# Optimization experiments

Hardware: AMD Instinct MI355X
Metric: run time of the kernel (lower is better)

Reference implementation:

```python
import jax, jax.numpy as jnp
import numpy as np
from jax import lax

WS = 11
CH = 3
DENOM_G = 2 * 0.2 ** 2
DENOM_L = 2 * 0.2 ** 2
C1 = 0.01 ** 2
C2 = 0.03 ** 2


def _make_window(ws=WS, channel=CH):
    sigma = ws / 6.0
    x = np.arange(ws) - ws // 2
    g = np.exp(-(x ** 2) / (2.0 * sigma ** 2))
    g = g / g.sum()
    w2 = np.outer(g, g)  # [ws, ws]
    w = np.broadcast_to(w2, (1, channel, ws, ws)) / channel  # sum over channels, averaged
    return jnp.asarray(w, dtype=jnp.float32)


def _wconv(x, window):
    # x: [N, C, H, W] -> [N, 1, H, W], SAME padding (ws odd)
    pad = WS // 2
    return lax.conv_general_dilated(
        x, window, window_strides=(1, 1), padding=[(pad, pad), (pad, pad)],
        dimension_numbers=("NCHW", "OIHW", "NCHW"))


def setup_inputs() -> dict:
    key = jax.random.key(0)
    k1, k2 = jax.random.split(key)
    X = jax.random.uniform(k1, (1, CH, 2048, 2048), dtype=jnp.float32)
    Ys = jax.random.uniform(k2, (4, CH, 2048, 2048), dtype=jnp.float32)
    return {"X": X, "Ys": Ys}


def reference(X, Ys):
    K, C, H, W = Ys.shape
    window = _make_window(WS, C)

    muY_seq = _wconv(Ys, window).reshape(K, H, W)
    sigmaY_sq_seq = _wconv(Ys * Ys, window).reshape(K, H, W) - muY_seq * muY_seq
    patch_index = jnp.argmax(sigmaY_sq_seq, axis=0)  # [H, W]

    muX = _wconv(X, window).reshape(H, W)
    muX_sq = muX * muX
    sigmaX_sq = _wconv(X * X, window).reshape(H, W) - muX_sq
    sigmaXY = _wconv(X * Ys, window).reshape(K, H, W) - muX[None] * muY_seq

    cs_seq = (2 * sigmaXY + C2) / (sigmaX_sq[None] + sigmaY_sq_seq + C2)  # [K, H, W]
    cs_map = jnp.take_along_axis(cs_seq, patch_index[None], axis=0)[0]  # [H, W]

    # is_lum=True luminance component
    lY = jnp.mean(muY_seq.reshape(K, -1), axis=1)  # [K]
    lL = jnp.exp(-((muY_seq - 0.5) ** 2) / DENOM_L)  # [K, H, W]
    lG = jnp.exp(-((lY - 0.5) ** 2) / DENOM_G)[:, None, None]  # [K, 1, 1]
    LY = lG * lL
    muY = jnp.sum(LY * muY_seq, axis=0) / jnp.sum(LY, axis=0)  # [H, W]
    l_map = (2 * muX * muY + C1) / (muX_sq + muY * muY + C1)

    q = jnp.mean(l_map * cs_map)
    return q
```

## Files before the change

kernel.cpp:

```cpp
#include <hip/hip_runtime.h>
#include <math.h>

#define HH 2048
#define WW 2048
#define PLANE 4194304
#define TPITCH 44
#define TPP (26*TPITCH)


__device__ inline double wave_red(double v) {
#pragma unroll
  for (int o = 32; o > 0; o >>= 1) v += __shfl_down(v, o, 64);
  return v;
}

__global__ void k0_window(float* gwin, float* gwin3) {
  if (threadIdx.x == 0) {
    double e[11], s = 0.0;
    double sig = 11.0 / 6.0;
    for (int i = 0; i < 11; ++i) {
      double x = (double)(i - 5);
      e[i] = exp(-(x * x) / (2.0 * sig * sig));
      s += e[i];
    }
    for (int i = 0; i < 11; ++i) {
      gwin[i]  = (float)(e[i] / s);
      gwin3[i] = (float)(e[i] / (3.0 * s));
    }
  }
}

__global__ __launch_bounds__(256) void k1_lY(const float* __restrict__ Ys,
                                             const float* __restrict__ gwin,
                                             double* __restrict__ lYpart) {
  int bid = blockIdx.x;
  int tid = threadIdx.x;
  double acc = 0.0;
  __shared__ float P[12];
  __shared__ double red[4];

  if (bid < 2048) {
    const float4* __restrict__ p = (const float4*)Ys;
    int base = bid * 6144 + tid;
#pragma unroll 1
    for (int gblk = 0; gblk < 3; ++gblk) {
      float ax = 0.f, ay = 0.f;
#pragma unroll
      for (int u = 0; u < 8; ++u) {
        float4 v = p[base + (gblk * 8 + u) * 256];
        ax += v.x + v.z;
        ay += v.y + v.w;
      }
      acc += (double)(ax + ay);
    }
  } else {
    int b = bid - 2048;
    int k = b >> 4, sub = b & 15;
    if (tid == 0) {
      float s = 0.f;
      for (int i = 0; i < 12; ++i) { P[i] = s; if (i < 11) s += gwin[i]; }
    }
    __syncthreads();
    const float4* __restrict__ Yk4 = (const float4*)(Ys + (size_t)k * 3 * PLANE);
    auto covP = [&](int r) -> float {
      if (r >= 5 && r <= 2042) return 1.0f;
      int dhi = r + 5; if (dhi > 10) dhi = 10;
      int dlo = r - 2042; if (dlo < 0) dlo = 0;
      return P[dhi + 1] - P[dlo];
    };
#pragma unroll 1
    for (int t = sub * 256 + tid; t < 39816; t += 4096) {
      int ch, row, g4;
      if (t < 15360) {
        ch = t / 5120;
        int r = (t % 5120) / 512;
        g4 = t & 511;
        row = (r < 5) ? r : r + 2038;
      } else {
        int u = t - 15360;
        ch = u / 8152;
        int rem = u % 8152;
        row = 5 + (rem >> 2);
        int gi = rem & 3;
        g4 = (gi < 2) ? gi : 508 + gi;
      }
      float4 v = Yk4[ch * 1048576 + row * 512 + g4];
      float cy = covP(row);
      int x0 = g4 << 2;
      float w0 = cy * covP(x0)     - 1.0f;
      float w1 = cy * covP(x0 + 1) - 1.0f;
      float w2 = cy * covP(x0 + 2) - 1.0f;
      float w3 = cy * covP(x0 + 3) - 1.0f;
      acc += (double)(w0 * v.x + w1 * v.y + w2 * v.z + w3 * v.w);
    }
  }

  acc = wave_red(acc);
  int lane = tid & 63, wid = tid >> 6;
  if (bid >= 2048 && tid == 0) {}
  __syncthreads();
  if (lane == 0) red[wid] = acc;
  __syncthreads();
  if (tid == 0) {
    double tot = red[0] + red[1] + red[2] + red[3];
    if (bid < 2048) {
      int k = bid >> 9;
      lYpart[k * 528 + (bid & 511)] = tot;
    } else {
      int b = bid - 2048;
      lYpart[(b >> 4) * 528 + 512 + (b & 15)] = tot;
    }
  }
}

__global__ __launch_bounds__(256) void k2a_lG(const double* __restrict__ lYpart,
                                              double* __restrict__ lG) {
  __shared__ double red[4];
  for (int k = 0; k < 4; ++k) {
    const double* p = lYpart + k * 528;
    double v = p[threadIdx.x] + p[256 + threadIdx.x];
    if (threadIdx.x < 16) v += p[512 + threadIdx.x];
    v = wave_red(v);
    int lane = threadIdx.x & 63, wid = threadIdx.x >> 6;
    if (lane == 0) red[wid] = v;
    __syncthreads();
    if (threadIdx.x == 0) {
      double tot = red[0] + red[1] + red[2] + red[3];
      double lY = tot * (1.0 / 12582912.0);
      double d = lY - 0.5;
      lG[k] = exp(-(d * d) / 0.08);
    }
    __syncthreads();
  }
}

__global__ __launch_bounds__(512, 4) void k2_main(const float* __restrict__ X,
                                                  const float* __restrict__ Ys,
                                                  const float* __restrict__ gwin,
                                                  const float* __restrict__ gwin3,
                                                  const double* __restrict__ lG,
                                                  double* __restrict__ qpart) {
  __shared__ float4 lds4[(4 + 14 * TPP) / 4];
  __shared__ double qred[8];
  float* prod = (float*)lds4 + 4;

  int bid = blockIdx.x;
  int wg = (bid & 7) * 1024 + (bid >> 3);
  int tX = wg & 63, tY = wg >> 6;
  int x0 = tX * 32, y0 = tY * 16;
  int tid = threadIdx.x;

  float g[11], g3[11];
#pragma unroll
  for (int i = 0; i < 11; ++i) { g[i] = gwin[i]; g3[i] = gwin3[i]; }

  if (tid < 286) {
    int row = tid / 11, g4 = tid - row * 11;
    int gy = y0 - 5 + row;
    int gx = x0 - 6 + g4 * 4;
    bool rok = (unsigned)gy < (unsigned)HH;
    size_t rbase = (size_t)gy * WW;
    float v[15][4];
#pragma unroll
    for (int p = 0; p < 15; ++p) {
      const float* src = (p < 3) ? (X + (size_t)p * PLANE)
                                 : (Ys + (size_t)(p - 3) * PLANE);
#pragma unroll
      for (int h = 0; h < 2; ++h) {
        int xx = gx + 2 * h;
        float2 w2 = make_float2(0.f, 0.f);
        if (rok && (unsigned)xx < (unsigned)WW)
          w2 = *(const float2*)(src + rbase + xx);
        v[p][2 * h] = w2.x;
        v[p][2 * h + 1] = w2.y;
      }
    }
    int ob = row * TPITCH + g4 * 4;
    {
      float4 a, b2;
#pragma unroll
      for (int e = 0; e < 4; ++e) {
        float s0 = v[0][e], s1 = v[1][e], s2 = v[2][e];
        ((float*)&a)[e]  = s0 + s1 + s2;
        ((float*)&b2)[e] = s0 * s0 + s1 * s1 + s2 * s2;
      }
      *(float4*)(prod + 0 * TPP + ob) = a;
      *(float4*)(prod + 1 * TPP + ob) = b2;
#pragma unroll
      for (int k = 0; k < 4; ++k) {
        float4 sy, sy2, sxy;
#pragma unroll
        for (int e = 0; e < 4; ++e) {
          float ya = v[3 + 3 * k][e], yb = v[4 + 3 * k][e], yc = v[5 + 3 * k][e];
          ((float*)&sy)[e]  = ya + yb + yc;
          ((float*)&sy2)[e] = ya * ya + yb * yb + yc * yc;
          ((float*)&sxy)[e] = v[0][e] * ya + v[1][e] * yb + v[2][e] * yc;
        }
        *(float4*)(prod + (2 + k) * TPP + ob)  = sy;
        *(float4*)(prod + (6 + k) * TPP + ob)  = sy2;
        *(float4*)(prod + (10 + k) * TPP + ob) = sxy;
      }
    }
  }
  __syncthreads();

  if (tid < 364) {
    int f = tid / 26, row = tid - f * 26;
    float* rp = prod + f * TPP + row * TPITCH;
    float w[44];
#pragma unroll
    for (int j = 0; j < 11; ++j) {
      float4 w4 = *(const float4*)(rp + 4 * j);
      w[4 * j] = w4.x; w[4 * j + 1] = w4.y; w[4 * j + 2] = w4.z; w[4 * j + 3] = w4.w;
    }
#pragma unroll
    for (int gq = 0; gq < 9; ++gq) {
      float4 o4;
#pragma unroll
      for (int e = 0; e < 4; ++e) {
        int p = 4 * gq + e;
        float s = 0.f;
#pragma unroll
        for (int d = 0; d < 11; ++d) {
          int wi = p - 1 + d;
          if (wi < 0) wi = 0;
          if (wi > 43) wi = 43;
          s += g[d] * w[wi];
        }
        ((float*)&o4)[e] = s;
      }
      *(float4*)(rp + 4 + 4 * gq) = o4;
    }
  }
  __syncthreads();

  float4 cacc[8];
  int cf = 0, ccg = 0, chalf = 0;
  bool cvalid = tid < 252;
  if (cvalid) {
    int t = tid;
    cf = t / 18;
    int r = t - cf * 18;
    ccg = 1 + (r >> 1);
    chalf = r & 1;
    const float* cp = prod + cf * TPP + (chalf * 8) * TPITCH + ccg * 4;
#pragma unroll
    for (int i = 0; i < 8; ++i) cacc[i] = make_float4(0.f, 0.f, 0.f, 0.f);
#pragma unroll
    for (int j = 0; j < 18; ++j) {
      float4 vv = *(const float4*)(cp + j * TPITCH);
#pragma unroll
      for (int r2 = 0; r2 < 8; ++r2) {
        int d = j - r2;
        if (d >= 0 && d < 11) {
          cacc[r2].x += g3[d] * vv.x;
          cacc[r2].y += g3[d] * vv.y;
          cacc[r2].z += g3[d] * vv.z;
          cacc[r2].w += g3[d] * vv.w;
        }
      }
    }
  }
  __syncthreads();
  if (cvalid) {
    float* cp = prod + cf * TPP + (chalf * 8) * TPITCH + ccg * 4;
#pragma unroll
    for (int r2 = 0; r2 < 8; ++r2)
      *(float4*)(cp + r2 * TPITCH) = cacc[r2];
  }
  __syncthreads();

  {
    int ty = tid >> 5, tx = tid & 31;
    int o = ty * TPITCH + 6 + tx;
    float b[14];
#pragma unroll
    for (int f = 0; f < 14; ++f) b[f] = prod[f * TPP + o];
    float muX = b[0];
    float muX2 = muX * muX;
    float sigX = b[1] - muX2;
    float num = 0.f, den = 0.f;
    float best_sig = -1e30f, best_cs = 0.f;
#pragma unroll
    for (int k = 0; k < 4; ++k) {
      float muY  = b[2 + k];
      float sigY = b[6 + k] - muY * muY;
      float sXY  = b[10 + k] - muX * muY;
      float cs = (2.f * sXY + 9e-4f) / (sigX + sigY + 9e-4f);
      if (sigY > best_sig) { best_sig = sigY; best_cs = cs; }
      float dm = muY - 0.5f;
      float lL = expf(-dm * dm * 12.5f);
      float LY = (float)lG[k] * lL;
      num += LY * muY;
      den += LY;
    }
    float muYw = num / den;
    float l = (2.f * muX * muYw + 1e-4f) / (muX2 + muYw * muYw + 1e-4f);
    double v = (double)(l * best_cs);
    v = wave_red(v);
    int lane = tid & 63, wid = tid >> 6;
    if (lane == 0) qred[wid] = v;
    __syncthreads();
    if (tid == 0) {
      double t = 0.0;
#pragma unroll
      for (int i = 0; i < 8; ++i) t += qred[i];
      qpart[blockIdx.x] = t;
    }
  }
}

__global__ __launch_bounds__(512) void k3_final(const double* __restrict__ qpart,
                                                float* __restrict__ out) {
  double acc = 0.0;
  for (int i = threadIdx.x; i < 8192; i += 512) acc += qpart[i];
  acc = wave_red(acc);
  __shared__ double red[8];
  int lane = threadIdx.x & 63, wid = threadIdx.x >> 6;
  if (lane == 0) red[wid] = acc;
  __syncthreads();
  if (threadIdx.x == 0)
    out[0] = (float)((red[0] + red[1] + red[2] + red[3] +
                      red[4] + red[5] + red[6] + red[7]) * (1.0 / 4194304.0));
}

extern "C" void kernel_launch(void* const* d_in, const int* in_sizes, int n_in,
                              void* d_out, int out_size, void* d_ws, size_t ws_size,
                              hipStream_t stream) {
  const float* X  = (const float*)d_in[0];
  const float* Ys = (const float*)d_in[1];
  char* ws = (char*)d_ws;
  float*  gwin   = (float*)(ws + 0);
  float*  gwin3  = (float*)(ws + 64);
  double* lG     = (double*)(ws + 128);
  double* lYpart = (double*)(ws + 256);
  double* qpart  = (double*)(ws + 17408);
  float* out = (float*)d_out;

  hipLaunchKernelGGL(k0_window, dim3(1), dim3(64), 0, stream, gwin, gwin3);
  hipLaunchKernelGGL(k1_lY, dim3(2112), dim3(256), 0, stream, Ys, gwin, lYpart);
  hipLaunchKernelGGL(k2a_lG, dim3(1), dim3(256), 0, stream, lYpart, lG);
  hipLaunchKernelGGL(k2_main, dim3(8192), dim3(512), 0, stream, X, Ys, gwin, gwin3, lG, qpart);
  hipLaunchKernelGGL(k3_final, dim3(1), dim3(512), 0, stream, qpart, out);
}
```

Baseline: 171.0 us.

## Split X and Y conv passes to shrink LDS tile and raise occupancy

The main kernel now convolves the two X feature planes first, keeps muX and sigX in registers, and then reuses the same LDS region for the twelve Y-derived planes. This cuts shared memory per block from fourteen planes to twelve. The tile height drops from 16 to 15 rows so each tile fits 25 halo rows, and launch bounds are raised to 6 blocks per CU. The aim is higher occupancy, paid for with an extra pass of barriers, a second read of X from global memory, more blocks (8768), and masking of the partial bottom tile.

```diff
diff --git a/kernel.cpp b/kernel.cpp
--- a/kernel.cpp
+++ b/kernel.cpp
@@ -4,8 +4,11 @@
 #define HH 2048
 #define WW 2048
 #define PLANE 4194304
+#define TROWS 25
 #define TPITCH 44
-#define TPP (26*TPITCH)
+#define TPP (TROWS*TPITCH)
+#define NBLK 8768
+#define CHUNK 1096
 
 
 __device__ inline double wave_red(double v) {
@@ -97,7 +100,6 @@
 
   acc = wave_red(acc);
   int lane = tid & 63, wid = tid >> 6;
-  if (bid >= 2048 && tid == 0) {}
   __syncthreads();
   if (lane == 0) red[wid] = acc;
   __syncthreads();
@@ -134,32 +136,140 @@
   }
 }
 
-__global__ __launch_bounds__(512, 4) void k2_main(const float* __restrict__ X,
+#define HB_BODY(NP) do {                                                   \
+    if (tid < (NP) * TROWS) {                                              \
+      int hf = tid / TROWS, hrow = tid - hf * TROWS;                       \
+      float* rp = lds + hf * TPP + hrow * TPITCH;                          \
+      float w[44];                                                         \
+      _Pragma("unroll")                                                    \
+      for (int j = 0; j < 11; ++j) {                                       \
+        float4 w4 = *(const float4*)(rp + 4 * j);                          \
+        w[4*j] = w4.x; w[4*j+1] = w4.y; w[4*j+2] = w4.z; w[4*j+3] = w4.w;  \
+      }                                                                    \
+      _Pragma("unroll")                                                    \
+      for (int gq = 0; gq < 9; ++gq) {                                     \
+        float4 o4;                                                         \
+        _Pragma("unroll")                                                  \
+        for (int e = 0; e < 4; ++e) {                                      \
+          int pp = 4 * gq + e;                                             \
+          float s = 0.f;                                                   \
+          _Pragma("unroll")                                                \
+          for (int d = 0; d < 11; ++d) {                                   \
+            int wi = pp - 1 + d;                                           \
+            if (wi < 0) wi = 0;                                            \
+            if (wi > 43) wi = 43;                                          \
+            s += g[d] * w[wi];                                             \
+          }                                                                \
+          ((float*)&o4)[e] = s;                                            \
+        }                                                                  \
+        *(float4*)(rp + 4 + 4 * gq) = o4;                                  \
+      }                                                                    \
+    }                                                                      \
+  } while (0)
+
+#define VB_BODY(NP) do {                                                   \
+    float4 vacc[8];                                                        \
+    bool vvalid = tid < (NP) * 18;                                         \
+    int vf = 0, vcg = 0, vrb = 0;                                          \
+    if (vvalid) {                                                          \
+      vf = tid / 18;                                                       \
+      int rr = tid - vf * 18;                                              \
+      vcg = 1 + (rr >> 1);                                                 \
+      vrb = (rr & 1) * 7;                                                  \
+      const float* cp = lds + vf * TPP + vrb * TPITCH + vcg * 4;           \
+      _Pragma("unroll")                                                    \
+      for (int i = 0; i < 8; ++i) vacc[i] = make_float4(0.f, 0.f, 0.f, 0.f); \
+      _Pragma("unroll")                                                    \
+      for (int j = 0; j < 18; ++j) {                                       \
+        float4 vv = *(const float4*)(cp + j * TPITCH);                     \
+        _Pragma("unroll")                                                  \
+        for (int r2 = 0; r2 < 8; ++r2) {                                   \
+          int d = j - r2;                                                  \
+          if (d >= 0 && d < 11) {                                          \
+            vacc[r2].x += g3[d] * vv.x;                                    \
+            vacc[r2].y += g3[d] * vv.y;                                    \
+            vacc[r2].z += g3[d] * vv.z;                                    \
+            vacc[r2].w += g3[d] * vv.w;                                    \
+          }                                                                \
+        }                                                                  \
+      }                                                                    \
+    }                                                                      \
+    __syncthreads();                                                       \
+    if (vvalid) {                                                          \
+      float* wp = lds + vf * TPP + vrb * TPITCH + vcg * 4;                 \
+      _Pragma("unroll")                                                    \
+      for (int r2 = 0; r2 < 8; ++r2)                                       \
+        *(float4*)(wp + r2 * TPITCH) = vacc[r2];                           \
+    }                                                                      \
+  } while (0)
+
+__global__ __launch_bounds__(512, 6) void k2_main(const float* __restrict__ X,
                                                   const float* __restrict__ Ys,
                                                   const float* __restrict__ gwin,
                                                   const float* __restrict__ gwin3,
                                                   const double* __restrict__ lG,
                                                   double* __restrict__ qpart) {
-  __shared__ float4 lds4[(4 + 14 * TPP) / 4];
+  __shared__ float4 lds4[12 * TPP / 4];
   __shared__ double qred[8];
-  float* prod = (float*)lds4 + 4;
+  float* lds = (float*)lds4;
 
   int bid = blockIdx.x;
-  int wg = (bid & 7) * 1024 + (bid >> 3);
+  int wg = (bid & 7) * CHUNK + (bid >> 3);
   int tX = wg & 63, tY = wg >> 6;
-  int x0 = tX * 32, y0 = tY * 16;
+  int x0 = tX * 32, y0 = tY * 15;
   int tid = threadIdx.x;
 
   float g[11], g3[11];
 #pragma unroll
   for (int i = 0; i < 11; ++i) { g[i] = gwin[i]; g3[i] = gwin3[i]; }
 
-  if (tid < 286) {
-    int row = tid / 11, g4 = tid - row * 11;
-    int gy = y0 - 5 + row;
-    int gx = x0 - 6 + g4 * 4;
-    bool rok = (unsigned)gy < (unsigned)HH;
-    size_t rbase = (size_t)gy * WW;
+  int arow = tid / 11, ag = tid - arow * 11;
+  int agy = y0 - 5 + arow;
+  int agx = x0 - 6 + 4 * ag;
+  bool aactive = tid < 275;
+  bool arok = aactive && ((unsigned)agy < (unsigned)HH);
+  size_t arbase = arok ? (size_t)agy * WW : 0;
+  int aob = arow * TPITCH + 4 * ag;
+
+  int dty = tid >> 5, dtx = tid & 31;
+  int doff = dty * TPITCH + 6 + dtx;
+  bool dvalid = (dty < 15) && (y0 + dty < HH);
+
+  if (aactive) {
+    float v[3][4];
+#pragma unroll
+    for (int p = 0; p < 3; ++p) {
+      const float* src = X + (size_t)p * PLANE;
+#pragma unroll
+      for (int h = 0; h < 2; ++h) {
+        int xx = agx + 2 * h;
+        float2 w2 = make_float2(0.f, 0.f);
+        if (arok && (unsigned)xx < (unsigned)WW)
+          w2 = *(const float2*)(src + arbase + xx);
+        v[p][2 * h] = w2.x;
+        v[p][2 * h + 1] = w2.y;
+      }
+    }
+    float4 sx, sx2;
+#pragma unroll
+    for (int e = 0; e < 4; ++e) {
+      float s0 = v[0][e], s1 = v[1][e], s2 = v[2][e];
+      ((float*)&sx)[e]  = s0 + s1 + s2;
+      ((float*)&sx2)[e] = s0 * s0 + s1 * s1 + s2 * s2;
+    }
+    *(float4*)(lds + 0 * TPP + aob) = sx;
+    *(float4*)(lds + 1 * TPP + aob) = sx2;
+  }
+  __syncthreads();
+  HB_BODY(2);
+  __syncthreads();
+  VB_BODY(2);
+  __syncthreads();
+  float muX  = lds[0 * TPP + doff];
+  float sigX = lds[1 * TPP + doff] - muX * muX;
+  __syncthreads();
+
+  if (aactive) {
     float v[15][4];
 #pragma unroll
     for (int p = 0; p < 15; ++p) {
@@ -167,125 +277,47 @@
                                  : (Ys + (size_t)(p - 3) * PLANE);
 #pragma unroll
       for (int h = 0; h < 2; ++h) {
-        int xx = gx + 2 * h;
+        int xx = agx + 2 * h;
         float2 w2 = make_float2(0.f, 0.f);
-        if (rok && (unsigned)xx < (unsigned)WW)
-          w2 = *(const float2*)(src + rbase + xx);
+        if (arok && (unsigned)xx < (unsigned)WW)
+          w2 = *(const float2*)(src + arbase + xx);
         v[p][2 * h] = w2.x;
         v[p][2 * h + 1] = w2.y;
       }
     }
-    int ob = row * TPITCH + g4 * 4;
-    {
-      float4 a, b2;
+#pragma unroll
+    for (int k = 0; k < 4; ++k) {
+      float4 sy, sy2, sxy;
 #pragma unroll
       for (int e = 0; e < 4; ++e) {
-        float s0 = v[0][e], s1 = v[1][e], s2 = v[2][e];
-        ((float*)&a)[e]  = s0 + s1 + s2;
-        ((float*)&b2)[e] = s0 * s0 + s1 * s1 + s2 * s2;
-      }
-      *(float4*)(prod + 0 * TPP + ob) = a;
-      *(float4*)(prod + 1 * TPP + ob) = b2;
-#pragma unroll
-      for (int k = 0; k < 4; ++k) {
-        float4 sy, sy2, sxy;
-#pragma unroll
-        for (int e = 0; e < 4; ++e) {
-          float ya = v[3 + 3 * k][e], yb = v[4 + 3 * k][e], yc = v[5 + 3 * k][e];
-          ((float*)&sy)[e]  = ya + yb + yc;
-          ((float*)&sy2)[e] = ya * ya + yb * yb + yc * yc;
-          ((float*)&sxy)[e] = v[0][e] * ya + v[1][e] * yb + v[2][e] * yc;
-        }
-        *(float4*)(prod + (2 + k) * TPP + ob)  = sy;
-        *(float4*)(prod + (6 + k) * TPP + ob)  = sy2;
-        *(float4*)(prod + (10 + k) * TPP + ob) = sxy;
-      }
-    }
-  }
-  __syncthreads();
-
-  if (tid < 364) {
-    int f = tid / 26, row = tid - f * 26;
-    float* rp = prod + f * TPP + row * TPITCH;
-    float w[44];
-#pragma unroll
-    for (int j = 0; j < 11; ++j) {
-      float4 w4 = *(const float4*)(rp + 4 * j);
-      w[4 * j] = w4.x; w[4 * j + 1] = w4.y; w[4 * j + 2] = w4.z; w[4 * j + 3] = w4.w;
-    }
-#pragma unroll
-    for (int gq = 0; gq < 9; ++gq) {
-      float4 o4;
-#pragma unroll
-      for (int e = 0; e < 4; ++e) {
-        int p = 4 * gq + e;
-        float s = 0.f;
-#pragma unroll
-        for (int d = 0; d < 11; ++d) {
-          int wi = p - 1 + d;
-          if (wi < 0) wi = 0;
-          if (wi > 43) wi = 43;
-          s += g[d] * w[wi];
-        }
-        ((float*)&o4)[e] = s;
-      }
-      *(float4*)(rp + 4 + 4 * gq) = o4;
-    }
-  }
-  __syncthreads();
-
-  float4 cacc[8];
-  int cf = 0, ccg = 0, chalf = 0;
-  bool cvalid = tid < 252;
-  if (cvalid) {
-    int t = tid;
-    cf = t / 18;
-    int r = t - cf * 18;
-    ccg = 1 + (r >> 1);
-    chalf = r & 1;
-    const float* cp = prod + cf * TPP + (chalf * 8) * TPITCH + ccg * 4;
-#pragma unroll
-    for (int i = 0; i < 8; ++i) cacc[i] = make_float4(0.f, 0.f, 0.f, 0.f);
-#pragma unroll
-    for (int j = 0; j < 18; ++j) {
-      float4 vv = *(const float4*)(cp + j * TPITCH);
-#pragma unroll
-      for (int r2 = 0; r2 < 8; ++r2) {
-        int d = j - r2;
-        if (d >= 0 && d < 11) {
-          cacc[r2].x += g3[d] * vv.x;
-          cacc[r2].y += g3[d] * vv.y;
-          cacc[r2].z += g3[d] * vv.z;
-          cacc[r2].w += g3[d] * vv.w;
-        }
-      }
-    }
-  }
-  __syncthreads();
-  if (cvalid) {
-    float* cp = prod + cf * TPP + (chalf * 8) * TPITCH + ccg * 4;
-#pragma unroll
-    for (int r2 = 0; r2 < 8; ++r2)
-      *(float4*)(cp + r2 * TPITCH) = cacc[r2];
-  }
+        float ya = v[3 + 3 * k][e], yb = v[4 + 3 * k][e], yc = v[5 + 3 * k][e];
+        ((float*)&sy)[e]  = ya + yb + yc;
+        ((float*)&sy2)[e] = ya * ya + yb * yb + yc * yc;
+        ((float*)&sxy)[e] = v[0][e] * ya + v[1][e] * yb + v[2][e] * yc;
+      }
+      *(float4*)(lds + (3 * k + 0) * TPP + aob) = sy;
+      *(float4*)(lds + (3 * k + 1) * TPP + aob) = sy2;
+      *(float4*)(lds + (3 * k + 2) * TPP + aob) = sxy;
+    }
+  }
+  __syncthreads();
+  HB_BODY(12);
+  __syncthreads();
+  VB_BODY(12);
   __syncthreads();
 
   {
-    int ty = tid >> 5, tx = tid & 31;
-    int o = ty * TPITCH + 6 + tx;
-    float b[14];
-#pragma unroll
-    for (int f = 0; f < 14; ++f) b[f] = prod[f * TPP + o];
-    float muX = b[0];
+    float b[12];
+#pragma unroll
+    for (int f = 0; f < 12; ++f) b[f] = lds[f * TPP + doff];
     float muX2 = muX * muX;
-    float sigX = b[1] - muX2;
     float num = 0.f, den = 0.f;
     float best_sig = -1e30f, best_cs = 0.f;
 #pragma unroll
     for (int k = 0; k < 4; ++k) {
-      float muY  = b[2 + k];
-      float sigY = b[6 + k] - muY * muY;
-      float sXY  = b[10 + k] - muX * muY;
+      float muY  = b[3 * k];
+      float sigY = b[3 * k + 1] - muY * muY;
+      float sXY  = b[3 * k + 2] - muX * muY;
       float cs = (2.f * sXY + 9e-4f) / (sigX + sigY + 9e-4f);
       if (sigY > best_sig) { best_sig = sigY; best_cs = cs; }
       float dm = muY - 0.5f;
@@ -296,7 +328,7 @@
     }
     float muYw = num / den;
     float l = (2.f * muX * muYw + 1e-4f) / (muX2 + muYw * muYw + 1e-4f);
-    double v = (double)(l * best_cs);
+    double v = dvalid ? (double)(l * best_cs) : 0.0;
     v = wave_red(v);
     int lane = tid & 63, wid = tid >> 6;
     if (lane == 0) qred[wid] = v;
@@ -313,7 +345,7 @@
 __global__ __launch_bounds__(512) void k3_final(const double* __restrict__ qpart,
                                                 float* __restrict__ out) {
   double acc = 0.0;
-  for (int i = threadIdx.x; i < 8192; i += 512) acc += qpart[i];
+  for (int i = threadIdx.x; i < NBLK; i += 512) acc += qpart[i];
   acc = wave_red(acc);
   __shared__ double red[8];
   int lane = threadIdx.x & 63, wid = threadIdx.x >> 6;
@@ -340,6 +372,6 @@
   hipLaunchKernelGGL(k0_window, dim3(1), dim3(64), 0, stream, gwin, gwin3);
   hipLaunchKernelGGL(k1_lY, dim3(2112), dim3(256), 0, stream, Ys, gwin, lYpart);
   hipLaunchKernelGGL(k2a_lG, dim3(1), dim3(256), 0, stream, lYpart, lG);
-  hipLaunchKernelGGL(k2_main, dim3(8192), dim3(512), 0, stream, X, Ys, gwin, gwin3, lG, qpart);
+  hipLaunchKernelGGL(k2_main, dim3(NBLK), dim3(512), 0, stream, X, Ys, gwin, gwin3, lG, qpart);
   hipLaunchKernelGGL(k3_final, dim3(1), dim3(512), 0, stream, qpart, out);
 }
```

Result: slower. 188.8 us (+10.4%).
